# Kernel tuning notes

Measured on AMD Instinct MI355X. Metric: run time of the kernel, lower is better.

The kernel has to match this reference:

```python
import jax, jax.numpy as jnp
import numpy as np

B, C, H, W = 8, 256, 48, 48


def setup_inputs() -> dict:
    key = jax.random.key(0)
    k1, k2, k3 = jax.random.split(key, 3)
    x = jax.random.normal(k1, (B, C, H, W), dtype=jnp.float32)
    # torch zero-inits W; we randomize (scaled) so the output is non-trivial
    W_w = jax.random.normal(k2, (C, C), dtype=jnp.float32) * 0.02
    W_b = jax.random.normal(k3, (C,), dtype=jnp.float32) * 0.02
    return {"x": x, "W_w": W_w, "W_b": W_b}


def reference(x, W_w, W_b):
    b, c, h, w = x.shape
    xf = x.reshape(b, c, h * w)                      # (b, C, N), N = H*W
    # f = theta_x @ phi_x = X^T X  -> (b, N, N)
    f = jnp.einsum('bcn,bcm->bnm', xf, xf)
    p = jax.nn.softmax(f, axis=-1)                   # (b, N, N)
    # y = p @ g_x where g_x = X^T -> (b, N, C); store as (b, C, N)
    y = jnp.einsum('bnm,bcm->bcn', p, xf).reshape(b, c, h, w)
    # 1x1 conv W + bias, then residual
    W_y = jnp.einsum('oc,bchw->bohw', W_w, y) + W_b[None, :, None, None]
    return W_y + x
```

## Files before the change

### kernel.cpp

```cpp
#include <hip/hip_runtime.h>
#include <stdint.h>

#define BATCH 8
#define CH    256
#define NN    2304
#define KVB   32

typedef __bf16 bf16x8 __attribute__((ext_vector_type(8)));
typedef float  f32x4  __attribute__((ext_vector_type(4)));
typedef unsigned short u16x8 __attribute__((ext_vector_type(8)));
typedef unsigned int   u32x4 __attribute__((ext_vector_type(4)));

static __device__ inline unsigned short f2bf(float f) {
    __bf16 h = (__bf16)f;
    return __builtin_bit_cast(unsigned short, h);
}
static __device__ inline unsigned pk2(float a, float b) {
    return (unsigned)f2bf(a) | ((unsigned)f2bf(b) << 16);
}
static __device__ inline float bf2f(unsigned short u) {
    unsigned v = (unsigned)u << 16;
    return __builtin_bit_cast(float, v);
}

#define GLOAD_LDS(gp, lp) __builtin_amdgcn_global_load_lds( \
    (const __attribute__((address_space(1))) unsigned int*)(gp), \
    (__attribute__((address_space(3))) unsigned int*)(lp), 16, 0, 0)

__global__ __launch_bounds__(256) void ktrans(
    const float* __restrict__ x, const float* __restrict__ Ww,
    unsigned short* __restrict__ Xt, unsigned short* __restrict__ Wbf)
{
    const int bid = blockIdx.x;
    const int t   = threadIdx.x;
    const int TPB = 4 * 36;
    if (bid >= BATCH * TPB) {
        const int wb = bid - BATCH * TPB;
        const int base = wb * 8192 + t;
        #pragma unroll
        for (int i = 0; i < 32; ++i)
            Wbf[base + i * 256] = f2bf(Ww[base + i * 256]);
        return;
    }
    const int b    = bid / TPB;
    const int tile = bid % TPB;
    const int c0   = (tile / 36) * 64;
    const int n0   = (tile % 36) * 64;
    __shared__ float ld[64][65];
    {
        const int row = t >> 2, seg = t & 3;
        const float* src = x + ((size_t)b * CH + c0 + row) * NN + n0 + seg * 16;
        #pragma unroll
        for (int q = 0; q < 4; ++q) {
            float4 v = *reinterpret_cast<const float4*>(src + q * 4);
            ld[row][seg * 16 + q * 4 + 0] = v.x;
            ld[row][seg * 16 + q * 4 + 1] = v.y;
            ld[row][seg * 16 + q * 4 + 2] = v.z;
            ld[row][seg * 16 + q * 4 + 3] = v.w;
        }
    }
    __syncthreads();
    {
        const int j = t >> 2, cs = t & 3;
        u16x8 v0, v1;
        #pragma unroll
        for (int k = 0; k < 8; ++k) v0[k] = f2bf(ld[cs * 16 + k][j]);
        #pragma unroll
        for (int k = 0; k < 8; ++k) v1[k] = f2bf(ld[cs * 16 + 8 + k][j]);
        unsigned short* dst = Xt + ((size_t)b * NN + n0 + j) * CH + c0 + cs * 16;
        *reinterpret_cast<u16x8*>(dst)     = v0;
        *reinterpret_cast<u16x8*>(dst + 8) = v1;
    }
}

__global__ __launch_bounds__(256) void kconv(
    const unsigned short* __restrict__ Xt,
    const unsigned short* __restrict__ Wb,
    unsigned short* __restrict__ Zc)
{
    const int bid  = blockIdx.x;
    const int b    = bid & 7;
    const int rest = bid >> 3;
    const int ot   = rest / 9;
    const int nt   = rest % 9;
    const int tid  = threadIdx.x;
    const int lane = tid & 63, w = tid >> 6;
    const int lr = lane & 15, lg = lane >> 4;
    const int ob = ot * 64;
    const int nb = nt * 256 + w * 64;

    f32x4 acc[4][4];
    f32x4 z = {0.f, 0.f, 0.f, 0.f};
    #pragma unroll
    for (int og = 0; og < 4; ++og)
        #pragma unroll
        for (int ng = 0; ng < 4; ++ng) acc[og][ng] = z;

    const unsigned short* wp = Wb + (size_t)(ob + lr) * CH + lg * 8;
    const unsigned short* xp = Xt + ((size_t)b * NN + nb + lr) * CH + lg * 8;
    #pragma unroll 1
    for (int kc = 0; kc < 8; ++kc) {
        bf16x8 af[4], bf[4];
        #pragma unroll
        for (int og = 0; og < 4; ++og)
            af[og] = *reinterpret_cast<const bf16x8*>(wp + (size_t)og * 16 * CH + kc * 32);
        #pragma unroll
        for (int ng = 0; ng < 4; ++ng)
            bf[ng] = *reinterpret_cast<const bf16x8*>(xp + (size_t)ng * 16 * CH + kc * 32);
        #pragma unroll
        for (int og = 0; og < 4; ++og)
            #pragma unroll
            for (int ng = 0; ng < 4; ++ng)
                acc[og][ng] = __builtin_amdgcn_mfma_f32_16x16x32_bf16(af[og], bf[ng], acc[og][ng], 0, 0, 0);
    }
    #pragma unroll
    for (int og = 0; og < 4; ++og)
        #pragma unroll
        for (int ng = 0; ng < 4; ++ng)
            #pragma unroll
            for (int r = 0; r < 4; ++r)
                Zc[((size_t)b * CH + ob + og * 16 + lg * 4 + r) * NN + nb + ng * 16 + lr] =
                    f2bf(acc[og][ng][r]);
}

static __device__ inline bf16x8 packP(f32x4 s0, f32x4 s1, float sd, float& lsum,
                                      int lr, int lg) {
    float p0[4], p1[4];
    #pragma unroll
    for (int r = 0; r < 4; ++r) {
        p0[r] = __expf(s0[r] - sd);
        p1[r] = __expf(s1[r] - sd);
        lsum += p0[r] + p1[r];
    }
    unsigned u0 = pk2(p0[0], p0[1]), u1 = pk2(p0[2], p0[3]);
    unsigned u2 = pk2(p1[0], p1[1]), u3 = pk2(p1[2], p1[3]);
    int s0l = lr + ((lg & 1) << 5);
    unsigned a0 = (unsigned)__shfl((int)u0, s0l),      c0 = (unsigned)__shfl((int)u2, s0l);
    unsigned a1 = (unsigned)__shfl((int)u1, s0l),      c1 = (unsigned)__shfl((int)u3, s0l);
    unsigned a2 = (unsigned)__shfl((int)u0, s0l + 16), c2 = (unsigned)__shfl((int)u2, s0l + 16);
    unsigned a3 = (unsigned)__shfl((int)u1, s0l + 16), c3 = (unsigned)__shfl((int)u3, s0l + 16);
    bool hi = (lg >= 2);
    u32x4 pw;
    pw[0] = hi ? c0 : a0;
    pw[1] = hi ? c1 : a1;
    pw[2] = hi ? c2 : a2;
    pw[3] = hi ? c3 : a3;
    return __builtin_bit_cast(bf16x8, pw);
}

__global__ __launch_bounds__(256, 2) void kattn(
    const unsigned short* __restrict__ Xt,
    const unsigned short* __restrict__ Zc,
    unsigned short* __restrict__ pA,
    float* __restrict__ pL,
    int hshift)
{
    __shared__ __attribute__((aligned(16))) unsigned char smem[2][32768];

    const int bid  = blockIdx.x;
    const int b    = bid & 7;
    const int r    = bid >> 3;
    const int qt   = r >> hshift;
    const int h    = r & ((1 << hshift) - 1);
    const int kvh  = NN >> hshift;
    const int nit  = kvh >> 5;
    const int tid  = threadIdx.x;
    const int lane = tid & 63;
    const int w    = tid >> 6;
    const int lr = lane & 15;
    const int lg = lane >> 4;
    const int qbase = qt * 128 + w * 32;

    const unsigned short* xtb = Xt + (size_t)b * NN * CH;
    const char* kSrc = (const char*)xtb + (size_t)h * kvh * 512;
    const char* vSrc = (const char*)(Zc + (size_t)b * CH * NN) + (size_t)h * kvh * 2;

    int koff[4], voff[4];
    #pragma unroll
    for (int i = 0; i < 4; ++i) {
        int p = w * 4096 + i * 1024 + lane * 16;
        int krow = p >> 9, kc_ = p & 511;
        koff[i] = krow * 512 + (kc_ ^ ((krow & 15) << 4));
        int o = p >> 6, vc = p & 63;
        voff[i] = o * 4608 + (vc ^ (((o >> 1) & 3) << 4));
    }

    bf16x8 qa0[8], qa1[8];
    {
        const unsigned short* qp0 = xtb + (size_t)(qbase + lr) * CH + lg * 8;
        const unsigned short* qp1 = xtb + (size_t)(qbase + 16 + lr) * CH + lg * 8;
        #pragma unroll
        for (int kc = 0; kc < 8; ++kc) {
            qa0[kc] = *reinterpret_cast<const bf16x8*>(qp0 + kc * 32);
            qa1[kc] = *reinterpret_cast<const bf16x8*>(qp1 + kc * 32);
        }
    }
    float sd0 = 0.f, sd1 = 0.f;
    #pragma unroll
    for (int kc = 0; kc < 8; ++kc)
        #pragma unroll
        for (int j = 0; j < 8; ++j) {
            float v0 = (float)qa0[kc][j];
            float v1 = (float)qa1[kc][j];
            sd0 = fmaf(v0, v0, sd0);
            sd1 = fmaf(v1, v1, sd1);
        }
    sd0 += __shfl_xor(sd0, 16); sd0 += __shfl_xor(sd0, 32);
    sd1 += __shfl_xor(sd1, 16); sd1 += __shfl_xor(sd1, 32);

    f32x4 acc0[16], acc1[16];
    f32x4 zz = {0.f, 0.f, 0.f, 0.f};
    #pragma unroll
    for (int og = 0; og < 16; ++og) { acc0[og] = zz; acc1[og] = zz; }
    float ls0 = 0.f, ls1 = 0.f;

    const int kx = lr << 4;
    const int vx = (lg * 16) ^ (((lr >> 1) & 3) << 4);

    {
        unsigned char* kb = &smem[0][w * 4096];
        unsigned char* vb = &smem[0][16384 + w * 4096];
        #pragma unroll
        for (int i = 0; i < 4; ++i) GLOAD_LDS(kSrc + koff[i], kb + i * 1024);
        #pragma unroll
        for (int i = 0; i < 4; ++i) GLOAD_LDS(vSrc + voff[i], vb + i * 1024);
    }
    __syncthreads();

    int cur = 0;
    #pragma unroll 1
    for (int ti = 0; ti < nit; ++ti) {
        if (ti + 1 < nit) {
            const char* ks = kSrc + (size_t)(ti + 1) * KVB * 512;
            const char* vs = vSrc + (size_t)(ti + 1) * KVB * 2;
            unsigned char* kb = &smem[cur ^ 1][w * 4096];
            unsigned char* vb = &smem[cur ^ 1][16384 + w * 4096];
            #pragma unroll
            for (int i = 0; i < 4; ++i) GLOAD_LDS(ks + koff[i], kb + i * 1024);
            #pragma unroll
            for (int i = 0; i < 4; ++i) GLOAD_LDS(vs + voff[i], vb + i * 1024);
        }

        const unsigned char* kbuf = smem[cur];
        const unsigned char* vbuf = smem[cur] + 16384;

        f32x4 s00 = zz, s01 = zz, s10 = zz, s11 = zz;
        #pragma unroll
        for (int kc = 0; kc < 8; ++kc) {
            bf16x8 k0 = *reinterpret_cast<const bf16x8*>(kbuf + lr * 512        + ((lg * 16 + kc * 64) ^ kx));
            bf16x8 k1 = *reinterpret_cast<const bf16x8*>(kbuf + lr * 512 + 8192 + ((lg * 16 + kc * 64) ^ kx));
            s00 = __builtin_amdgcn_mfma_f32_16x16x32_bf16(k0, qa0[kc], s00, 0, 0, 0);
            s01 = __builtin_amdgcn_mfma_f32_16x16x32_bf16(k1, qa0[kc], s01, 0, 0, 0);
            s10 = __builtin_amdgcn_mfma_f32_16x16x32_bf16(k0, qa1[kc], s10, 0, 0, 0);
            s11 = __builtin_amdgcn_mfma_f32_16x16x32_bf16(k1, qa1[kc], s11, 0, 0, 0);
        }

        bf16x8 pb0 = packP(s00, s01, sd0, ls0, lr, lg);
        bf16x8 pb1 = packP(s10, s11, sd1, ls1, lr, lg);

        #pragma unroll
        for (int og = 0; og < 16; ++og) {
            bf16x8 vb = *reinterpret_cast<const bf16x8*>(vbuf + (og * 16 + lr) * 64 + vx);
            acc0[og] = __builtin_amdgcn_mfma_f32_16x16x32_bf16(vb, pb0, acc0[og], 0, 0, 0);
            acc1[og] = __builtin_amdgcn_mfma_f32_16x16x32_bf16(vb, pb1, acc1[og], 0, 0, 0);
        }

        __syncthreads();
        cur ^= 1;
    }

    ls0 += __shfl_xor(ls0, 16); ls0 += __shfl_xor(ls0, 32);
    ls1 += __shfl_xor(ls1, 16); ls1 += __shfl_xor(ls1, 32);

    if (lg == 0) {
        pL[(size_t)(h * 8 + b) * NN + qbase + lr]      = ls0;
        pL[(size_t)(h * 8 + b) * NN + qbase + 16 + lr] = ls1;
    }
    const size_t pbase = (size_t)(h * 8 + b) * 256;
    #pragma unroll
    for (int og = 0; og < 16; ++og) {
        #pragma unroll
        for (int rr = 0; rr < 4; ++rr) {
            const int o = og * 16 + lg * 4 + rr;
            pA[(pbase + o) * NN + qbase + lr]      = f2bf(acc0[og][rr]);
            pA[(pbase + o) * NN + qbase + 16 + lr] = f2bf(acc1[og][rr]);
        }
    }
}

__global__ __launch_bounds__(256) void kmerge(
    const unsigned short* __restrict__ pA, const float* __restrict__ pL,
    const float* __restrict__ x, const float* __restrict__ bias,
    float* __restrict__ out, int nsplit)
{
    const int b = blockIdx.x >> 8;
    const int o = blockIdx.x & 255;
    const float bo = bias[o];
    const size_t xb = ((size_t)b * 256 + o) * NN;
    #pragma unroll
    for (int k = 0; k < 9; ++k) {
        const int n = k * 256 + threadIdx.x;
        float v = 0.f, l = 0.f;
        for (int c = 0; c < nsplit; ++c) {
            v += bf2f(pA[(((size_t)(c * 8 + b)) * 256 + o) * NN + n]);
            l += pL[((size_t)(c * 8 + b)) * NN + n];
        }
        out[xb + n] = v / l + bo + x[xb + n];
    }
}

extern "C" void kernel_launch(void* const* d_in, const int* in_sizes, int n_in,
                              void* d_out, int out_size, void* d_ws, size_t ws_size,
                              hipStream_t stream) {
    const float* x    = (const float*)d_in[0];
    const float* Ww   = (const float*)d_in[1];
    const float* bias = (const float*)d_in[2];
    float* out = (float*)d_out;

    unsigned short* Xt  = (unsigned short*)d_ws;
    unsigned short* Zc  = Xt + (size_t)BATCH * NN * CH;
    unsigned short* Wbf = Zc + (size_t)BATCH * NN * CH;
    unsigned short* pA  = Wbf + (size_t)CH * CH;
    float*          pL  = (float*)(pA + (size_t)4 * BATCH * CH * NN);

    const size_t need4 = (size_t)9437184 * 2 + 131072
                       + (size_t)4 * BATCH * CH * NN * 2
                       + (size_t)4 * BATCH * NN * 4;
    int nsplit, hshift;
    if (ws_size >= need4) { nsplit = 4; hshift = 2; }
    else                  { nsplit = 2; hshift = 1;
        pL = (float*)(pA + (size_t)2 * BATCH * CH * NN); }

    ktrans<<<8 * 144 + 8,       256, 0, stream>>>(x, Ww, Xt, Wbf);
    kconv <<<288,               256, 0, stream>>>(Xt, Wbf, Zc);
    kattn <<<8 * 18 * nsplit,   256, 0, stream>>>(Xt, Zc, pA, pL, hshift);
    kmerge<<<2048,              256, 0, stream>>>(pA, pL, x, bias, out, nsplit);
}
```

Measured before the change: 125.4 us.

## Single-buffer attention LDS, pack partial outputs as bf16 pairs, allow 8-way KV split

Replaces the double-buffered K/V shared-memory pipeline with a single 32KB buffer and an extra barrier per tile, halving LDS use so more workgroups can be resident per CU. Partial attention outputs are now stored as packed 32-bit bf16 pairs (acc0/acc1 interleaved), giving fewer, wider stores, and kmerge unpacks them with matching indexing. The KV split can now go to 8 when workspace allows, launching more blocks at the cost of more merge traffic. Losing prefetch overlap exposes global load latency unless occupancy hides it.

```diff
diff --git a/kernel.cpp b/kernel.cpp
--- a/kernel.cpp
+++ b/kernel.cpp
@@ -151,11 +151,11 @@
 __global__ __launch_bounds__(256, 2) void kattn(
     const unsigned short* __restrict__ Xt,
     const unsigned short* __restrict__ Zc,
-    unsigned short* __restrict__ pA,
+    unsigned* __restrict__ pA32,
     float* __restrict__ pL,
     int hshift)
 {
-    __shared__ __attribute__((aligned(16))) unsigned char smem[2][32768];
+    __shared__ __attribute__((aligned(16))) unsigned char smem[32768];
 
     const int bid  = blockIdx.x;
     const int b    = bid & 7;
@@ -218,8 +218,8 @@
     const int vx = (lg * 16) ^ (((lr >> 1) & 3) << 4);
 
     {
-        unsigned char* kb = &smem[0][w * 4096];
-        unsigned char* vb = &smem[0][16384 + w * 4096];
+        unsigned char* kb = &smem[w * 4096];
+        unsigned char* vb = &smem[16384 + w * 4096];
         #pragma unroll
         for (int i = 0; i < 4; ++i) GLOAD_LDS(kSrc + koff[i], kb + i * 1024);
         #pragma unroll
@@ -227,22 +227,10 @@
     }
     __syncthreads();
 
-    int cur = 0;
     #pragma unroll 1
     for (int ti = 0; ti < nit; ++ti) {
-        if (ti + 1 < nit) {
-            const char* ks = kSrc + (size_t)(ti + 1) * KVB * 512;
-            const char* vs = vSrc + (size_t)(ti + 1) * KVB * 2;
-            unsigned char* kb = &smem[cur ^ 1][w * 4096];
-            unsigned char* vb = &smem[cur ^ 1][16384 + w * 4096];
-            #pragma unroll
-            for (int i = 0; i < 4; ++i) GLOAD_LDS(ks + koff[i], kb + i * 1024);
-            #pragma unroll
-            for (int i = 0; i < 4; ++i) GLOAD_LDS(vs + voff[i], vb + i * 1024);
-        }
-
-        const unsigned char* kbuf = smem[cur];
-        const unsigned char* vbuf = smem[cur] + 16384;
+        const unsigned char* kbuf = smem;
+        const unsigned char* vbuf = smem + 16384;
 
         f32x4 s00 = zz, s01 = zz, s10 = zz, s11 = zz;
         #pragma unroll
@@ -266,7 +254,17 @@
         }
 
         __syncthreads();
-        cur ^= 1;
+        if (ti + 1 < nit) {
+            const char* ks = kSrc + (size_t)(ti + 1) * KVB * 512;
+            const char* vs = vSrc + (size_t)(ti + 1) * KVB * 2;
+            unsigned char* kb = &smem[w * 4096];
+            unsigned char* vb = &smem[16384 + w * 4096];
+            #pragma unroll
+            for (int i = 0; i < 4; ++i) GLOAD_LDS(ks + koff[i], kb + i * 1024);
+            #pragma unroll
+            for (int i = 0; i < 4; ++i) GLOAD_LDS(vs + voff[i], vb + i * 1024);
+        }
+        __syncthreads();
     }
 
     ls0 += __shfl_xor(ls0, 16); ls0 += __shfl_xor(ls0, 32);
@@ -276,20 +274,20 @@
         pL[(size_t)(h * 8 + b) * NN + qbase + lr]      = ls0;
         pL[(size_t)(h * 8 + b) * NN + qbase + 16 + lr] = ls1;
     }
-    const size_t pbase = (size_t)(h * 8 + b) * 256;
+    const size_t rowbase = (size_t)(h * 8 + b) * 256;
+    const int ub = (qbase >> 1) + lr;
     #pragma unroll
     for (int og = 0; og < 16; ++og) {
         #pragma unroll
         for (int rr = 0; rr < 4; ++rr) {
             const int o = og * 16 + lg * 4 + rr;
-            pA[(pbase + o) * NN + qbase + lr]      = f2bf(acc0[og][rr]);
-            pA[(pbase + o) * NN + qbase + 16 + lr] = f2bf(acc1[og][rr]);
+            pA32[(rowbase + o) * (NN / 2) + ub] = pk2(acc0[og][rr], acc1[og][rr]);
         }
     }
 }
 
 __global__ __launch_bounds__(256) void kmerge(
-    const unsigned short* __restrict__ pA, const float* __restrict__ pL,
+    const unsigned* __restrict__ pA32, const float* __restrict__ pL,
     const float* __restrict__ x, const float* __restrict__ bias,
     float* __restrict__ out, int nsplit)
 {
@@ -300,9 +298,12 @@
     #pragma unroll
     for (int k = 0; k < 9; ++k) {
         const int n = k * 256 + threadIdx.x;
+        const int ui = (n >> 5) * 16 + (n & 15);
+        const int hi = (n >> 4) & 1;
         float v = 0.f, l = 0.f;
         for (int c = 0; c < nsplit; ++c) {
-            v += bf2f(pA[(((size_t)(c * 8 + b)) * 256 + o) * NN + n]);
+            unsigned pv = pA32[(((size_t)(c * 8 + b)) * 256 + o) * (NN / 2) + ui];
+            v += bf2f((unsigned short)(hi ? (pv >> 16) : (pv & 0xffff)));
             l += pL[((size_t)(c * 8 + b)) * NN + n];
         }
         out[xb + n] = v / l + bo + x[xb + n];
@@ -320,19 +321,20 @@
     unsigned short* Xt  = (unsigned short*)d_ws;
     unsigned short* Zc  = Xt + (size_t)BATCH * NN * CH;
     unsigned short* Wbf = Zc + (size_t)BATCH * NN * CH;
-    unsigned short* pA  = Wbf + (size_t)CH * CH;
-    float*          pL  = (float*)(pA + (size_t)4 * BATCH * CH * NN);
-
-    const size_t need4 = (size_t)9437184 * 2 + 131072
-                       + (size_t)4 * BATCH * CH * NN * 2
-                       + (size_t)4 * BATCH * NN * 4;
-    int nsplit, hshift;
-    if (ws_size >= need4) { nsplit = 4; hshift = 2; }
-    else                  { nsplit = 2; hshift = 1;
-        pL = (float*)(pA + (size_t)2 * BATCH * CH * NN); }
+    unsigned*       pA32 = (unsigned*)(Wbf + (size_t)CH * CH);
+
+    const size_t base = (size_t)9437184 * 2 + 131072;
+    const size_t perSplit = (size_t)BATCH * CH * NN * 2
+                          + (size_t)BATCH * NN * 4;
+    int hshift;
+    if      (ws_size >= base + 8 * perSplit) hshift = 3;
+    else if (ws_size >= base + 4 * perSplit) hshift = 2;
+    else                                     hshift = 1;
+    const int nsplit = 1 << hshift;
+    float* pL = (float*)(pA32 + (size_t)nsplit * BATCH * CH * (NN / 2));
 
     ktrans<<<8 * 144 + 8,       256, 0, stream>>>(x, Ww, Xt, Wbf);
     kconv <<<288,               256, 0, stream>>>(Xt, Wbf, Zc);
-    kattn <<<8 * 18 * nsplit,   256, 0, stream>>>(Xt, Zc, pA, pL, hshift);
-    kmerge<<<2048,              256, 0, stream>>>(pA, pL, x, bias, out, nsplit);
-}
+    kattn <<<8 * 18 * nsplit,   256, 0, stream>>>(Xt, Zc, pA32, pL, hshift);
+    kmerge<<<2048,              256, 0, stream>>>(pA32, pL, x, bias, out, nsplit);
+}
```

Measured after the change: 129.2 us. 3.0% more time.
